# Performance work log

Hardware: AMD Instinct MI355X
Metric: run time of the kernel (lower is better)

The kernel has to match this reference:

```python
import jax, jax.numpy as jnp
import numpy as np

B, Z_DIM, T_DIM, ACT_E, CF, N_ACT, STEPS = 256, 256, 512, 256, 1024, 64, 64


def setup_inputs() -> dict:
    key = jax.random.key(0)
    ks = jax.random.split(key, 12)
    s = 0.02
    def n(k, shape):
        return jax.random.normal(k, shape, jnp.float32) * s
    return {
        "z": jax.random.normal(ks[0], (B, Z_DIM), jnp.float32),
        "W_z2t": n(ks[1], (T_DIM, Z_DIM)), "b_z2t": jnp.zeros((T_DIM,), jnp.float32),
        "E": n(ks[2], (N_ACT, ACT_E)),  # encoder_act2e embedding table
        "Wih_a": n(ks[3], (4 * CF, T_DIM + ACT_E)), "Whh_a": n(ks[4], (4 * CF, CF)),
        "bih_a": jnp.zeros((4 * CF,), jnp.float32), "bhh_a": jnp.zeros((4 * CF,), jnp.float32),
        "Wih_t": n(ks[5], (4 * CF, T_DIM + ACT_E + 1)), "Whh_t": n(ks[6], (4 * CF, CF)),
        "bih_t": jnp.zeros((4 * CF,), jnp.float32), "bhh_t": jnp.zeros((4 * CF,), jnp.float32),
        "W_act": n(ks[7], (N_ACT, CF)), "b_act": jnp.zeros((N_ACT,), jnp.float32),
        "W_ts1": n(ks[8], (CF // 2, CF)), "b_ts1": jnp.zeros((CF // 2,), jnp.float32),
        "W_ts2": n(ks[9], (1, CF // 2)), "b_ts2": jnp.zeros((1,), jnp.float32),
    }


def _lstm_step(x, h, c, Wih, Whh, bih, bhh):
    # PyTorch LSTM gate order: i, f, g, o
    gates = x @ Wih.T + h @ Whh.T + bih + bhh
    i, f, g, o = jnp.split(gates, 4, axis=-1)
    c = jax.nn.sigmoid(f) * c + jax.nn.sigmoid(i) * jnp.tanh(g)
    h = jax.nn.sigmoid(o) * jnp.tanh(c)
    return h, c


def reference(z, W_z2t, b_z2t, E, Wih_a, Whh_a, bih_a, bhh_a,
              Wih_t, Whh_t, bih_t, bhh_t, W_act, b_act,
              W_ts1, b_ts1, W_ts2, b_ts2):
    Bz = z.shape[0]
    t_rec = jax.nn.relu(z @ W_z2t.T + b_z2t)                 # [B, t_dim]
    zeros_h = jnp.zeros((Bz, CF), z.dtype)
    act_emb0 = jnp.broadcast_to(E[-1], (Bz, ACT_E))          # EOT token embedding
    ts0 = jnp.zeros((Bz, 1), z.dtype)

    def step(carry, _):
        h_a, c_a, h_t, c_t, act_emb, ts = carry
        x_a = jnp.concatenate([t_rec, act_emb], axis=1)       # [B, t_dim+act_e]
        h_a, c_a = _lstm_step(x_a, h_a, c_a, Wih_a, Whh_a, bih_a, bhh_a)
        logits = h_a @ W_act.T + b_act                        # [B, num_activities]
        act_emb = E[jnp.argmax(logits, axis=1)]               # [B, act_e]
        x_t = jnp.concatenate([t_rec, act_emb, ts], axis=1)   # [B, t_dim+act_e+1]
        h_t, c_t = _lstm_step(x_t, h_t, c_t, Wih_t, Whh_t, bih_t, bhh_t)
        ts = jax.nn.relu(h_t @ W_ts1.T + b_ts1) @ W_ts2.T + b_ts2  # [B, 1]
        return (h_a, c_a, h_t, c_t, act_emb, ts), (logits, ts)

    carry0 = (zeros_h, zeros_h, zeros_h, zeros_h, act_emb0, ts0)
    _, (logits_seq, ts_seq) = jax.lax.scan(step, carry0, None, length=STEPS)
    acts_rec = jax.nn.softmax(jnp.transpose(logits_seq, (1, 0, 2)), axis=2)  # [B, T, A]
    ts_rec = jnp.transpose(ts_seq[..., 0], (1, 0))                            # [B, T]
    return acts_rec, ts_rec
```

## Files before the change

kernel.cpp:

```cpp
#include <hip/hip_runtime.h>
#include <stdint.h>

typedef unsigned int u32;
typedef float  f32x4 __attribute__((ext_vector_type(4)));
typedef float  f32x2 __attribute__((ext_vector_type(2)));
typedef double f64x2 __attribute__((ext_vector_type(2)));
typedef double f64x4 __attribute__((ext_vector_type(4)));

constexpr int NT  = 256;
constexpr int NTA = 128;
constexpr int BB = 256;
constexpr int ZD = 256;
constexpr int TD = 512;
constexpr int CF = 1024;
constexpr int G4 = 4096;
constexpr int NA = 64;
constexpr int NSTEP = 64;
constexpr int TS_OFF = BB * NSTEP * NA;

constexpr int RSF = 34;
constexpr int FRS = 68;
constexpr int SMEMB = 2 * 64 * RSF * 8;

constexpr int ARS_A = 34;
constexpr int ASZ_A = 32 * ARS_A * 8;
constexpr int BSZ_A = 32 * ARS_A * 4;
constexpr int TRS   = 36;
constexpr int TSZ   = 32 * TRS * 4;
constexpr int SMEMA = (ASZ_A + BSZ_A) > (2 * TSZ) ? (ASZ_A + BSZ_A) : (2 * TSZ);

struct P {
  const float *z, *W_z2t, *b_z2t, *E, *Wih_a, *Whh_a, *bih_a, *bhh_a,
              *Wih_t, *Whh_t, *bih_t, *bhh_t, *W_act, *b_act, *W_ts1, *b_ts1, *W_ts2, *b_ts2;
  float* out;
  double *t_rec64, *pre_a64, *E_proj_a64, *h_a64, *c_a64, *gacc_a;
  float *t_rec32, *pre_t, *E_proj_t, *colt, *h_t, *c_t, *gacc_t, *ts_accum;
  int* idxb;
};

__device__ __forceinline__ float sigf(float x){ return 1.f / (1.f + expf(-x)); }
__device__ __forceinline__ float tanhf_(float x){
  float ax = fabsf(x); float e = expf(-2.f * ax);
  float t = 1.f - 2.f * e / (1.f + e);
  return x < 0.f ? -t : t;
}
__device__ __forceinline__ double sigd(double x){ return 1.0 / (1.0 + exp(-x)); }

__global__ void __launch_bounds__(NT) k_setup(P p){
  __shared__ double sz[ZD];
  const int bid = blockIdx.x, tid = threadIdx.x;
  for (int i = tid; i < ZD; i += NT) sz[i] = (double)p.z[bid * ZD + i];
  __syncthreads();
  for (int k = tid; k < TD; k += NT){
    const float* wr = p.W_z2t + (size_t)k * ZD;
    double a = 0.0;
    for (int j = 0; j < ZD; ++j) a = fma((double)wr[j], sz[j], a);
    a += (double)p.b_z2t[k];
    double t = a > 0.0 ? a : 0.0;
    p.t_rec64[(size_t)bid * TD + k] = t;
    p.t_rec32[(size_t)bid * TD + k] = (float)t;
  }
  for (int i = tid; i < CF; i += NT){
    p.c_a64[(size_t)bid * CF + i] = 0.0;
    p.h_a64[(size_t)bid * CF + i] = 0.0;
    p.c_t[(size_t)bid * CF + i] = 0.f;
    p.h_t[(size_t)bid * CF + i] = 0.f;
  }
  if (tid == 0){ p.idxb[bid] = NA - 1; p.ts_accum[bid] = 0.f; }
}

__global__ void __launch_bounds__(NT) k_eproj(P p){
  __shared__ double sz[ZD];
  const int bid = blockIdx.x, tid = threadIdx.x;
  if (bid < 256){
    const int erow = bid >> 2, cchunk = bid & 3;
    for (int i = tid; i < ZD; i += NT) sz[i] = (double)p.E[erow * ZD + i];
    __syncthreads();
    for (int ci = 0; ci < 4; ++ci){
      const int c = cchunk * 1024 + ci * 256 + tid;
      const float* wr = p.Wih_a + (size_t)c * 768 + 512;
      double a = 0.0;
      for (int j = 0; j < 256; ++j) a = fma((double)wr[j], sz[j], a);
      p.E_proj_a64[(size_t)erow * G4 + c] = a;
    }
  } else if (bid < 512){
    const int erow = (bid - 256) >> 2, cchunk = (bid - 256) & 3;
    for (int i = tid; i < ZD; i += NT) sz[i] = (double)p.E[erow * ZD + i];
    __syncthreads();
    for (int ci = 0; ci < 4; ++ci){
      const int c = cchunk * 1024 + ci * 256 + tid;
      const float* wr = p.Wih_t + (size_t)c * 769 + 512;
      float a = 0.f;
      for (int j = 0; j < 256; ++j) a = fmaf(wr[j], (float)sz[j], a);
      p.E_proj_t[(size_t)erow * G4 + c] = a;
    }
  } else {
    const int c = (bid - 512) * 256 + tid;
    p.colt[c] = p.Wih_t[(size_t)c * 769 + 768];
  }
}

template <bool A64, bool OUT64>
__device__ void mgemm64s(char* smem, const void* __restrict__ Av, int lda,
                         const float* __restrict__ B, int ldb,
                         int rowb, int colb, int K,
                         const float* __restrict__ bih, const float* __restrict__ bhh,
                         void* __restrict__ outv){
  double* As = (double*)smem;
  double* Bs = As + 64 * RSF;
  const int tid = threadIdx.x;
  const int lane = tid & 63;
  const int wm = (tid >> 7) & 1, wn = (tid >> 6) & 1;
  const int m = lane & 15, q = lane >> 4;
  const int tr = tid >> 2, tkq = tid & 3;
  const double* A64p = (const double*)Av;
  const float*  A32p = (const float*)Av;

  double av[8], bv[8];
  auto loadchunk = [&](int kb){
    if (A64){
      const double* ap = A64p + (size_t)(rowb + tr) * lda + kb + tkq * 8;
      #pragma unroll
      for (int j = 0; j < 8; ++j) av[j] = ap[j];
    } else {
      const float* ap = A32p + (size_t)(rowb + tr) * lda + kb + tkq * 8;
      #pragma unroll
      for (int j = 0; j < 8; ++j) av[j] = (double)ap[j];
    }
    const float* bp = B + (size_t)(colb + tr) * ldb + kb + tkq * 8;
    #pragma unroll
    for (int j = 0; j < 8; ++j) bv[j] = (double)bp[j];
  };
  f64x4 acc[2][2];
  #pragma unroll
  for (int g = 0; g < 2; ++g)
    #pragma unroll
    for (int h = 0; h < 2; ++h) acc[g][h] = f64x4{0.0,0.0,0.0,0.0};

  loadchunk(0);
  for (int kb = 0; kb < K; kb += 32){
    __syncthreads();
    {
      double* arow = As + tr * RSF + tkq * 8;
      double* brow = Bs + tr * RSF + tkq * 8;
      #pragma unroll
      for (int j = 0; j < 4; ++j){
        *(f64x2*)(arow + j * 2) = f64x2{av[j], av[j + 4]};
        *(f64x2*)(brow + j * 2) = f64x2{bv[j], bv[j + 4]};
      }
    }
    __syncthreads();
    if (kb + 32 < K) loadchunk(kb + 32);
    #pragma unroll
    for (int sp = 0; sp < 4; ++sp){
      const f64x2 a0 = *(const f64x2*)(As + (wm * 32 +  0 + m) * RSF + sp * 8 + q * 2);
      const f64x2 a1 = *(const f64x2*)(As + (wm * 32 + 16 + m) * RSF + sp * 8 + q * 2);
      const f64x2 b0 = *(const f64x2*)(Bs + (wn * 32 +  0 + m) * RSF + sp * 8 + q * 2);
      const f64x2 b1 = *(const f64x2*)(Bs + (wn * 32 + 16 + m) * RSF + sp * 8 + q * 2);
      acc[0][0] = __builtin_amdgcn_mfma_f64_16x16x4f64(a0[0], b0[0], acc[0][0], 0, 0, 0);
      acc[0][1] = __builtin_amdgcn_mfma_f64_16x16x4f64(a0[0], b1[0], acc[0][1], 0, 0, 0);
      acc[1][0] = __builtin_amdgcn_mfma_f64_16x16x4f64(a1[0], b0[0], acc[1][0], 0, 0, 0);
      acc[1][1] = __builtin_amdgcn_mfma_f64_16x16x4f64(a1[0], b1[0], acc[1][1], 0, 0, 0);
      acc[0][0] = __builtin_amdgcn_mfma_f64_16x16x4f64(a0[1], b0[1], acc[0][0], 0, 0, 0);
      acc[0][1] = __builtin_amdgcn_mfma_f64_16x16x4f64(a0[1], b1[1], acc[0][1], 0, 0, 0);
      acc[1][0] = __builtin_amdgcn_mfma_f64_16x16x4f64(a1[1], b0[1], acc[1][0], 0, 0, 0);
      acc[1][1] = __builtin_amdgcn_mfma_f64_16x16x4f64(a1[1], b1[1], acc[1][1], 0, 0, 0);
    }
  }
  #pragma unroll
  for (int g = 0; g < 2; ++g){
    const int rb = rowb + wm * 32 + g * 16 + q;
    #pragma unroll
    for (int h = 0; h < 2; ++h){
      const int cc = colb + wn * 32 + h * 16 + m;
      const double bb = (double)bih[cc] + (double)bhh[cc];
      #pragma unroll
      for (int v = 0; v < 4; ++v){
        if (OUT64) ((double*)outv)[(size_t)(rb + 4 * v) * G4 + cc] = acc[g][h][v] + bb;
        else       ((float*) outv)[(size_t)(rb + 4 * v) * G4 + cc] = (float)(acc[g][h][v] + bb);
      }
    }
  }
}

__device__ void dgemm32s(char* smem, const float* __restrict__ A, int lda,
                         const float* __restrict__ B, int ldb,
                         int rowb, int colb, int K,
                         const float* __restrict__ bih, const float* __restrict__ bhh,
                         float* __restrict__ outp){
  float* As = (float*)smem;
  float* Bs = (float*)(smem + 64 * FRS * 4);
  const int tid = threadIdx.x;
  const int tx = tid & 15, ty = tid >> 4;
  const int r_ = tid >> 2, kq = tid & 3;
  const int wsw = r_ ^ (kq * 8);
  float acc[4][4];
  #pragma unroll
  for (int i = 0; i < 4; ++i)
    #pragma unroll
    for (int j = 0; j < 4; ++j) acc[i][j] = 0.f;

  float pa[16], pb[16];
  auto ldA = [&](int kb){
    const float* ap = A + (size_t)(rowb + r_) * lda + kb + kq * 16;
    #pragma unroll
    for (int j = 0; j < 16; ++j) pa[j] = ap[j];
  };
  auto ldB = [&](int kb){
    const float* bp = B + (size_t)(colb + r_) * ldb + kb + kq * 16;
    #pragma unroll
    for (int j = 0; j < 16; ++j) pb[j] = bp[j];
  };
  ldA(0); ldB(0);
  for (int kb = 0; kb < K; kb += 64){
    __syncthreads();
    #pragma unroll
    for (int j = 0; j < 16; ++j){
      As[(kq * 16 + j) * FRS + wsw] = pa[j];
      Bs[(kq * 16 + j) * FRS + wsw] = pb[j];
    }
    __syncthreads();
    if (kb + 64 < K){ ldA(kb + 64); ldB(kb + 64); }
    #pragma unroll 4
    for (int k = 0; k < 64; ++k){
      const int sw = (k >> 4) * 8;
      f32x4 a4 = *(const f32x4*)(As + k * FRS + ((4 * ty) ^ sw));
      f32x4 b4 = *(const f32x4*)(Bs + k * FRS + ((4 * tx) ^ sw));
      acc[0][0] = fmaf(a4[0], b4[0], acc[0][0]); acc[0][1] = fmaf(a4[0], b4[1], acc[0][1]);
      acc[0][2] = fmaf(a4[0], b4[2], acc[0][2]); acc[0][3] = fmaf(a4[0], b4[3], acc[0][3]);
      acc[1][0] = fmaf(a4[1], b4[0], acc[1][0]); acc[1][1] = fmaf(a4[1], b4[1], acc[1][1]);
      acc[1][2] = fmaf(a4[1], b4[2], acc[1][2]); acc[1][3] = fmaf(a4[1], b4[3], acc[1][3]);
      acc[2][0] = fmaf(a4[2], b4[0], acc[2][0]); acc[2][1] = fmaf(a4[2], b4[1], acc[2][1]);
      acc[2][2] = fmaf(a4[2], b4[2], acc[2][2]); acc[2][3] = fmaf(a4[2], b4[3], acc[2][3]);
      acc[3][0] = fmaf(a4[3], b4[0], acc[3][0]); acc[3][1] = fmaf(a4[3], b4[1], acc[3][1]);
      acc[3][2] = fmaf(a4[3], b4[2], acc[3][2]); acc[3][3] = fmaf(a4[3], b4[3], acc[3][3]);
    }
  }
  const int c0 = colb + 4 * tx;
  float bb0 = bih[c0+0] + bhh[c0+0], bb1 = bih[c0+1] + bhh[c0+1];
  float bb2 = bih[c0+2] + bhh[c0+2], bb3 = bih[c0+3] + bhh[c0+3];
  #pragma unroll
  for (int i = 0; i < 4; ++i){
    float* o = outp + (size_t)(rowb + 4 * ty + i) * G4 + c0;
    o[0] = acc[i][0] + bb0; o[1] = acc[i][1] + bb1;
    o[2] = acc[i][2] + bb2; o[3] = acc[i][3] + bb3;
  }
}

__device__ void mgemm64w(char* smem, const double* __restrict__ A, int lda,
                         const float* __restrict__ B, int ldb,
                         int rowb, int colb, int K,
                         const double* __restrict__ addin, double* __restrict__ outp){
  double* As = (double*)smem;
  float*  Bs = (float*)(smem + ASZ_A);
  const int tid = threadIdx.x, lane = tid & 63;
  const int w = tid >> 6;
  const int m = lane & 15, q = lane >> 4;
  const int tr = tid >> 2, tkq = tid & 3;
  double av[8]; float bv[8];
  auto loadchunk = [&](int kb){
    const double* ap = A + (size_t)(rowb + tr) * lda + kb + tkq * 8;
    #pragma unroll
    for (int j = 0; j < 8; ++j) av[j] = ap[j];
    const float* bp = B + (size_t)(colb + tr) * ldb + kb + tkq * 8;
    #pragma unroll
    for (int j = 0; j < 8; ++j) bv[j] = bp[j];
  };
  f64x4 acc0{0,0,0,0}, acc1{0,0,0,0};
  loadchunk(0);
  for (int kb = 0; kb < K; kb += 32){
    __syncthreads();
    {
      double* arow = As + tr * ARS_A + tkq * 8;
      float*  brow = Bs + tr * ARS_A + tkq * 8;
      #pragma unroll
      for (int j = 0; j < 4; ++j){
        *(f64x2*)(arow + j * 2) = f64x2{av[j], av[j + 4]};
        *(f32x2*)(brow + j * 2) = f32x2{bv[j], bv[j + 4]};
      }
    }
    __syncthreads();
    if (kb + 32 < K) loadchunk(kb + 32);
    #pragma unroll
    for (int sp = 0; sp < 4; ++sp){
      const f64x2 a0  = *(const f64x2*)(As + (16 * w + m) * ARS_A + sp * 8 + q * 2);
      const f32x2 b0f = *(const f32x2*)(Bs + ( 0 + m) * ARS_A + sp * 8 + q * 2);
      const f32x2 b1f = *(const f32x2*)(Bs + (16 + m) * ARS_A + sp * 8 + q * 2);
      acc0 = __builtin_amdgcn_mfma_f64_16x16x4f64(a0[0], (double)b0f[0], acc0, 0, 0, 0);
      acc1 = __builtin_amdgcn_mfma_f64_16x16x4f64(a0[0], (double)b1f[0], acc1, 0, 0, 0);
      acc0 = __builtin_amdgcn_mfma_f64_16x16x4f64(a0[1], (double)b0f[1], acc0, 0, 0, 0);
      acc1 = __builtin_amdgcn_mfma_f64_16x16x4f64(a0[1], (double)b1f[1], acc1, 0, 0, 0);
    }
  }
  const int rb = rowb + 16 * w + q;
  #pragma unroll
  for (int h = 0; h < 2; ++h){
    const f64x4 a = h ? acc1 : acc0;
    const int cc = colb + h * 16 + m;
    #pragma unroll
    for (int v = 0; v < 4; ++v){
      const size_t o = (size_t)(rb + 4 * v) * G4 + cc;
      outp[o] = a[v] + addin[o];
    }
  }
}

__device__ void dgemm32w(char* smem, const float* __restrict__ A, int lda,
                         const float* __restrict__ B, int ldb,
                         int rowb, int colb, int K,
                         const float* __restrict__ addin, float* __restrict__ outp){
  float* As = (float*)smem;
  float* Bs = (float*)(smem + TSZ);
  const int tid = threadIdx.x;
  const int tx = tid & 7, ty = tid >> 3;
  const int r_ = tid >> 2, kq = tid & 3;
  const int wsw = r_ ^ (kq * 8);
  float acc[2][4];
  #pragma unroll
  for (int i = 0; i < 2; ++i)
    #pragma unroll
    for (int j = 0; j < 4; ++j) acc[i][j] = 0.f;
  float pa[8], pb[8];
  auto ldAB = [&](int kb){
    const float* ap = A + (size_t)(rowb + r_) * lda + kb + kq * 8;
    #pragma unroll
    for (int j = 0; j < 8; ++j) pa[j] = ap[j];
    const float* bp = B + (size_t)(colb + r_) * ldb + kb + kq * 8;
    #pragma unroll
    for (int j = 0; j < 8; ++j) pb[j] = bp[j];
  };
  ldAB(0);
  for (int kb = 0; kb < K; kb += 32){
    __syncthreads();
    #pragma unroll
    for (int j = 0; j < 8; ++j){
      As[(kq * 8 + j) * TRS + wsw] = pa[j];
      Bs[(kq * 8 + j) * TRS + wsw] = pb[j];
    }
    __syncthreads();
    if (kb + 32 < K) ldAB(kb + 32);
    #pragma unroll 4
    for (int k = 0; k < 32; ++k){
      const int sw = (k >> 3) * 8;
      f32x2 a2 = *(const f32x2*)(As + k * TRS + ((2 * ty) ^ sw));
      f32x4 b4 = *(const f32x4*)(Bs + k * TRS + ((4 * tx) ^ sw));
      acc[0][0] = fmaf(a2[0], b4[0], acc[0][0]); acc[0][1] = fmaf(a2[0], b4[1], acc[0][1]);
      acc[0][2] = fmaf(a2[0], b4[2], acc[0][2]); acc[0][3] = fmaf(a2[0], b4[3], acc[0][3]);
      acc[1][0] = fmaf(a2[1], b4[0], acc[1][0]); acc[1][1] = fmaf(a2[1], b4[1], acc[1][1]);
      acc[1][2] = fmaf(a2[1], b4[2], acc[1][2]); acc[1][3] = fmaf(a2[1], b4[3], acc[1][3]);
    }
  }
  const int c0 = colb + 4 * tx;
  #pragma unroll
  for (int i = 0; i < 2; ++i){
    const size_t base = (size_t)(rowb + 2 * ty + i) * G4 + c0;
    const float* ai = addin + base;
    float* o = outp + base;
    o[0] = acc[i][0] + ai[0]; o[1] = acc[i][1] + ai[1];
    o[2] = acc[i][2] + ai[2]; o[3] = acc[i][3] + ai[3];
  }
}

__device__ void tshead_j(const P& p, int bid, int hbuf){
  const int tid = threadIdx.x;
  const int tm = bid >> 6, tjq = bid & 63;
  const int rowb = tm * 32;
  const int rt = tid >> 3, j8 = tid & 7;
  const int j = tjq * 8 + j8;
  const float* __restrict__ hr = p.h_t + (size_t)hbuf * BB * CF + (size_t)(rowb + rt) * CF;
  const float* __restrict__ wr = p.W_ts1 + (size_t)j * CF;
  float a0=0,a1=0,a2=0,a3=0;
  for (int k = 0; k < CF; k += 16){
    f32x4 h0 = *(const f32x4*)(hr + k),     h1 = *(const f32x4*)(hr + k + 4);
    f32x4 h2 = *(const f32x4*)(hr + k + 8), h3 = *(const f32x4*)(hr + k + 12);
    f32x4 w0 = *(const f32x4*)(wr + k),     w1 = *(const f32x4*)(wr + k + 4);
    f32x4 w2 = *(const f32x4*)(wr + k + 8), w3 = *(const f32x4*)(wr + k + 12);
    a0 = fmaf(h0[0],w0[0], fmaf(h0[1],w0[1], fmaf(h0[2],w0[2], fmaf(h0[3],w0[3], a0))));
    a1 = fmaf(h1[0],w1[0], fmaf(h1[1],w1[1], fmaf(h1[2],w1[2], fmaf(h1[3],w1[3], a1))));
    a2 = fmaf(h2[0],w2[0], fmaf(h2[1],w2[1], fmaf(h2[2],w2[2], fmaf(h2[3],w2[3], a2))));
    a3 = fmaf(h3[0],w3[0], fmaf(h3[1],w3[1], fmaf(h3[2],w3[2], fmaf(h3[3],w3[3], a3))));
  }
  float v = ((a0 + a1) + (a2 + a3)) + p.b_ts1[j];
  v = (v > 0.f ? v : 0.f) * p.W_ts2[j];
  v += __shfl_xor(v, 1, 64);
  v += __shfl_xor(v, 2, 64);
  v += __shfl_xor(v, 4, 64);
  if (j8 == 0) atomicAdd(p.ts_accum + rowb + rt, v);
}

__device__ void tshead_j128(const P& p, int bid, int hbuf){
  const int tid = threadIdx.x;
  const int tm = bid >> 7, tjq = bid & 127;
  const int rowb = tm * 32;
  const int rt = tid >> 2, j4 = tid & 3;
  const int j = tjq * 4 + j4;
  const float* __restrict__ hr = p.h_t + (size_t)hbuf * BB * CF + (size_t)(rowb + rt) * CF;
  const float* __restrict__ wr = p.W_ts1 + (size_t)j * CF;
  float a0=0,a1=0,a2=0,a3=0;
  for (int k = 0; k < CF; k += 16){
    f32x4 h0 = *(const f32x4*)(hr + k),     h1 = *(const f32x4*)(hr + k + 4);
    f32x4 h2 = *(const f32x4*)(hr + k + 8), h3 = *(const f32x4*)(hr + k + 12);
    f32x4 w0 = *(const f32x4*)(wr + k),     w1 = *(const f32x4*)(wr + k + 4);
    f32x4 w2 = *(const f32x4*)(wr + k + 8), w3 = *(const f32x4*)(wr + k + 12);
    a0 = fmaf(h0[0],w0[0], fmaf(h0[1],w0[1], fmaf(h0[2],w0[2], fmaf(h0[3],w0[3], a0))));
    a1 = fmaf(h1[0],w1[0], fmaf(h1[1],w1[1], fmaf(h1[2],w1[2], fmaf(h1[3],w1[3], a1))));
    a2 = fmaf(h2[0],w2[0], fmaf(h2[1],w2[1], fmaf(h2[2],w2[2], fmaf(h2[3],w2[3], a2))));
    a3 = fmaf(h3[0],w3[0], fmaf(h3[1],w3[1], fmaf(h3[2],w3[2], fmaf(h3[3],w3[3], a3))));
  }
  float v = ((a0 + a1) + (a2 + a3)) + p.b_ts1[j];
  v = (v > 0.f ? v : 0.f) * p.W_ts2[j];
  v += __shfl_xor(v, 1, 64);
  v += __shfl_xor(v, 2, 64);
  if (j4 == 0) atomicAdd(p.ts_accum + rowb + rt, v);
}

__global__ void __launch_bounds__(NT) k_pre(P p){
  __shared__ __align__(16) char smem[SMEMB];
  const int bid = blockIdx.x;
  const int hsel = bid >> 8, sub = bid & 255;
  const int rowb = (sub >> 6) * 64, colb = (sub & 63) * 64;
  if (hsel == 0)
    mgemm64s<true, true>(smem, p.t_rec64, TD, p.Wih_a, 768, rowb, colb, TD,
                         p.bih_a, p.bhh_a, p.pre_a64);
  else
    dgemm32s(smem, p.t_rec32, TD, p.Wih_t, 769, rowb, colb, TD,
             p.bih_t, p.bhh_t, p.pre_t);
}

__global__ void __launch_bounds__(NTA) k_stepA(P p, int s){
  __shared__ __align__(16) char smem[SMEMA];
  const int bid = blockIdx.x;
  if (s > 0 && bid < 1024) tshead_j128(p, bid, s & 1);
  const int hsel = bid >> 10, sub = bid & 1023;
  const int rowb = (sub >> 7) * 32, colb = (sub & 127) * 32;
  const int rd = s & 1;
  if (hsel == 0)
    mgemm64w(smem, p.h_a64 + (size_t)rd * BB * CF, CF, p.Whh_a, CF,
             rowb, colb, CF, p.pre_a64, p.gacc_a);
  else
    dgemm32w(smem, p.h_t + (size_t)rd * BB * CF, CF, p.Whh_t, CF,
             rowb, colb, CF, p.pre_t, p.gacc_t);
}

__global__ void __launch_bounds__(NT) k_stepB(P p, int s){
  __shared__ double shd[1092];
  const int b = blockIdx.x, tid = threadIdx.x;
  const int cur = (s + 1) & 1;
  int idxp = p.idxb[b];
  idxp = idxp < 0 ? 0 : (idxp > 63 ? 63 : idxp);
  {
    const double* ga = p.gacc_a + (size_t)b * G4;
    const double* ea = p.E_proj_a64 + (size_t)idxp * G4;
    const int c0 = tid * 4;
    #pragma unroll
    for (int jj = 0; jj < 4; ++jj){
      const int c = c0 + jj;
      double gi = ga[0*CF + c] + ea[0*CF + c];
      double gf = ga[1*CF + c] + ea[1*CF + c];
      double gg = ga[2*CF + c] + ea[2*CF + c];
      double go = ga[3*CF + c] + ea[3*CF + c];
      double cv = p.c_a64[(size_t)b * CF + c];
      double cn = sigd(gf) * cv + sigd(gi) * tanh(gg);
      double hn = sigd(go) * tanh(cn);
      p.c_a64[(size_t)b * CF + c] = cn;
      p.h_a64[(size_t)cur * BB * CF + (size_t)b * CF + c] = hn;
      shd[c] = hn;
    }
  }
  if (tid == 0) shd[1088] = (s == 0) ? 0.0 : ((double)p.ts_accum[b] + (double)p.b_ts2[0]);
  __syncthreads();
  {
    const int w = tid >> 6, l = tid & 63, l15 = l & 15, quad = l >> 4;
    const int a = w * 16 + l15;
    const float* wr = p.W_act + (size_t)a * CF + quad * 256;
    const double* hp = shd + quad * 256;
    double acc = 0.0;
    for (int kk = 0; kk < 256; kk += 4){
      acc = fma((double)wr[kk+0], hp[kk+0], acc);
      acc = fma((double)wr[kk+1], hp[kk+1], acc);
      acc = fma((double)wr[kk+2], hp[kk+2], acc);
      acc = fma((double)wr[kk+3], hp[kk+3], acc);
    }
    acc += __shfl_xor(acc, 16, 64);
    acc += __shfl_xor(acc, 32, 64);
    if (quad == 0) shd[1024 + a] = acc;
  }
  __syncthreads();
  if (tid < 64){
    double acc = shd[1024 + tid] + (double)p.b_act[tid];
    double m = acc;
    #pragma unroll
    for (int off = 32; off; off >>= 1) m = fmax(m, __shfl_xor(m, off, 64));
    unsigned long long ball = __ballot(acc == m);
    int idxv = __ffsll(ball) - 1;
    idxv = idxv < 0 ? 0 : (idxv > 63 ? 63 : idxv);
    double e = exp(acc - m);
    double ssum = e;
    #pragma unroll
    for (int off = 32; off; off >>= 1) ssum += __shfl_xor(ssum, off, 64);
    p.out[(size_t)b * (NSTEP * NA) + s * NA + tid] = (float)(e / ssum);
    if (tid == 0){
      p.idxb[b] = idxv;
      shd[1089] = (double)idxv;
      if (s > 0) p.out[TS_OFF + b * NSTEP + (s - 1)] = (float)shd[1088];
    }
  }
  __syncthreads();
  const float ts_val = (float)shd[1088];
  const int idxv = (int)shd[1089];
  const int c0 = tid * 4;
  const float* gb = p.gacc_t   + (size_t)b * G4;
  const float* eb = p.E_proj_t + (size_t)idxv * G4;
  f32x4 gi = *(const f32x4*)(gb + 0*CF + c0) + *(const f32x4*)(eb + 0*CF + c0) + ts_val * *(const f32x4*)(p.colt + 0*CF + c0);
  f32x4 gf = *(const f32x4*)(gb + 1*CF + c0) + *(const f32x4*)(eb + 1*CF + c0) + ts_val * *(const f32x4*)(p.colt + 1*CF + c0);
  f32x4 gg = *(const f32x4*)(gb + 2*CF + c0) + *(const f32x4*)(eb + 2*CF + c0) + ts_val * *(const f32x4*)(p.colt + 2*CF + c0);
  f32x4 go = *(const f32x4*)(gb + 3*CF + c0) + *(const f32x4*)(eb + 3*CF + c0) + ts_val * *(const f32x4*)(p.colt + 3*CF + c0);
  f32x4 cv = *(f32x4*)(p.c_t + (size_t)b * CF + c0);
  f32x4 cn, hn;
  #pragma unroll
  for (int jj = 0; jj < 4; ++jj){
    float cj = sigf(gf[jj]) * cv[jj] + sigf(gi[jj]) * tanhf_(gg[jj]);
    float hj = sigf(go[jj]) * tanhf_(cj);
    cn[jj] = cj; hn[jj] = hj;
  }
  *(f32x4*)(p.c_t + (size_t)b * CF + c0) = cn;
  *(f32x4*)(p.h_t + (size_t)cur * BB * CF + (size_t)b * CF + c0) = hn;
  __syncthreads();
  if (tid == 0) p.ts_accum[b] = 0.f;
}

__global__ void __launch_bounds__(NT) k_tsfin(P p){
  tshead_j(p, blockIdx.x, 0);
}
__global__ void __launch_bounds__(NT) k_tswrite(P p){
  p.out[TS_OFF + threadIdx.x * NSTEP + 63] = p.ts_accum[threadIdx.x] + p.b_ts2[0];
}

extern "C" void kernel_launch(void* const* d_in, const int* in_sizes, int n_in,
                              void* d_out, int out_size, void* d_ws, size_t ws_size,
                              hipStream_t stream){
  (void)in_sizes; (void)n_in; (void)out_size; (void)ws_size;
  P p;
  p.z     = (const float*)d_in[0];  p.W_z2t = (const float*)d_in[1];  p.b_z2t = (const float*)d_in[2];
  p.E     = (const float*)d_in[3];  p.Wih_a = (const float*)d_in[4];  p.Whh_a = (const float*)d_in[5];
  p.bih_a = (const float*)d_in[6];  p.bhh_a = (const float*)d_in[7];  p.Wih_t = (const float*)d_in[8];
  p.Whh_t = (const float*)d_in[9];  p.bih_t = (const float*)d_in[10]; p.bhh_t = (const float*)d_in[11];
  p.W_act = (const float*)d_in[12]; p.b_act = (const float*)d_in[13]; p.W_ts1 = (const float*)d_in[14];
  p.b_ts1 = (const float*)d_in[15]; p.W_ts2 = (const float*)d_in[16]; p.b_ts2 = (const float*)d_in[17];
  p.out = (float*)d_out;
  char* w = (char*)d_ws;
  size_t off = 0;
  auto alloc = [&](size_t bytes) -> void* { void* r = w + off; off += (bytes + 255) & ~(size_t)255; return r; };
  p.t_rec64    = (double*)alloc((size_t)BB * TD * 8);
  p.pre_a64    = (double*)alloc((size_t)BB * G4 * 8);
  p.E_proj_a64 = (double*)alloc((size_t)NA * G4 * 8);
  p.h_a64      = (double*)alloc((size_t)2 * BB * CF * 8);
  p.c_a64      = (double*)alloc((size_t)BB * CF * 8);
  p.gacc_a     = (double*)alloc((size_t)BB * G4 * 8);
  p.t_rec32    = (float*)alloc((size_t)BB * TD * 4);
  p.pre_t      = (float*)alloc((size_t)BB * G4 * 4);
  p.E_proj_t   = (float*)alloc((size_t)NA * G4 * 4);
  p.colt       = (float*)alloc((size_t)G4 * 4);
  p.h_t        = (float*)alloc((size_t)2 * BB * CF * 4);
  p.c_t        = (float*)alloc((size_t)BB * CF * 4);
  p.gacc_t     = (float*)alloc((size_t)BB * G4 * 4);
  p.ts_accum   = (float*)alloc((size_t)BB * 4);
  p.idxb       = (int*)  alloc((size_t)BB * 4);

  k_setup<<<dim3(256), dim3(NT), 0, stream>>>(p);
  k_eproj<<<dim3(528), dim3(NT), 0, stream>>>(p);
  k_pre  <<<dim3(512), dim3(NT), 0, stream>>>(p);
  for (int s = 0; s < NSTEP; ++s){
    k_stepA<<<dim3(2048), dim3(NTA), 0, stream>>>(p, s);
    k_stepB<<<dim3(256),  dim3(NT),  0, stream>>>(p, s);
  }
  k_tsfin  <<<dim3(512), dim3(NT), 0, stream>>>(p);
  k_tswrite<<<dim3(1),   dim3(NT), 0, stream>>>(p);
}
```

Before: 10.10 ms.

## Shrink recurrent GEMM row tiles to 16 and double stepA grid

Result: slower. 12.89 ms (+27.6%).

```diff
diff --git a/kernel.cpp b/kernel.cpp
--- a/kernel.cpp
+++ b/kernel.cpp
@@ -23,7 +23,7 @@
 constexpr int SMEMB = 2 * 64 * RSF * 8;
 
 constexpr int ARS_A = 34;
-constexpr int ASZ_A = 32 * ARS_A * 8;
+constexpr int ASZ_A = 16 * ARS_A * 8;
 constexpr int BSZ_A = 32 * ARS_A * 4;
 constexpr int TRS   = 36;
 constexpr int TSZ   = 32 * TRS * 4;
@@ -247,7 +247,7 @@
   }
 }
 
-__device__ void mgemm64w(char* smem, const double* __restrict__ A, int lda,
+__device__ void mgemm16w(char* smem, const double* __restrict__ A, int lda,
                          const float* __restrict__ B, int ldb,
                          int rowb, int colb, int K,
                          const double* __restrict__ addin, double* __restrict__ outp){
@@ -259,53 +259,51 @@
   const int tr = tid >> 2, tkq = tid & 3;
   double av[8]; float bv[8];
   auto loadchunk = [&](int kb){
-    const double* ap = A + (size_t)(rowb + tr) * lda + kb + tkq * 8;
-    #pragma unroll
-    for (int j = 0; j < 8; ++j) av[j] = ap[j];
+    if (tid < 64){
+      const double* ap = A + (size_t)(rowb + tr) * lda + kb + tkq * 8;
+      #pragma unroll
+      for (int j = 0; j < 8; ++j) av[j] = ap[j];
+    }
     const float* bp = B + (size_t)(colb + tr) * ldb + kb + tkq * 8;
     #pragma unroll
     for (int j = 0; j < 8; ++j) bv[j] = bp[j];
   };
-  f64x4 acc0{0,0,0,0}, acc1{0,0,0,0};
+  f64x4 acc{0,0,0,0};
   loadchunk(0);
   for (int kb = 0; kb < K; kb += 32){
     __syncthreads();
     {
-      double* arow = As + tr * ARS_A + tkq * 8;
-      float*  brow = Bs + tr * ARS_A + tkq * 8;
-      #pragma unroll
-      for (int j = 0; j < 4; ++j){
-        *(f64x2*)(arow + j * 2) = f64x2{av[j], av[j + 4]};
+      float* brow = Bs + tr * ARS_A + tkq * 8;
+      #pragma unroll
+      for (int j = 0; j < 4; ++j)
         *(f32x2*)(brow + j * 2) = f32x2{bv[j], bv[j + 4]};
+      if (tid < 64){
+        double* arow = As + tr * ARS_A + tkq * 8;
+        #pragma unroll
+        for (int j = 0; j < 4; ++j)
+          *(f64x2*)(arow + j * 2) = f64x2{av[j], av[j + 4]};
       }
     }
     __syncthreads();
     if (kb + 32 < K) loadchunk(kb + 32);
     #pragma unroll
     for (int sp = 0; sp < 4; ++sp){
-      const f64x2 a0  = *(const f64x2*)(As + (16 * w + m) * ARS_A + sp * 8 + q * 2);
-      const f32x2 b0f = *(const f32x2*)(Bs + ( 0 + m) * ARS_A + sp * 8 + q * 2);
-      const f32x2 b1f = *(const f32x2*)(Bs + (16 + m) * ARS_A + sp * 8 + q * 2);
-      acc0 = __builtin_amdgcn_mfma_f64_16x16x4f64(a0[0], (double)b0f[0], acc0, 0, 0, 0);
-      acc1 = __builtin_amdgcn_mfma_f64_16x16x4f64(a0[0], (double)b1f[0], acc1, 0, 0, 0);
-      acc0 = __builtin_amdgcn_mfma_f64_16x16x4f64(a0[1], (double)b0f[1], acc0, 0, 0, 0);
-      acc1 = __builtin_amdgcn_mfma_f64_16x16x4f64(a0[1], (double)b1f[1], acc1, 0, 0, 0);
-    }
-  }
-  const int rb = rowb + 16 * w + q;
-  #pragma unroll
-  for (int h = 0; h < 2; ++h){
-    const f64x4 a = h ? acc1 : acc0;
-    const int cc = colb + h * 16 + m;
-    #pragma unroll
-    for (int v = 0; v < 4; ++v){
-      const size_t o = (size_t)(rb + 4 * v) * G4 + cc;
-      outp[o] = a[v] + addin[o];
-    }
-  }
-}
-
-__device__ void dgemm32w(char* smem, const float* __restrict__ A, int lda,
+      const f64x2 a0  = *(const f64x2*)(As + m * ARS_A + sp * 8 + q * 2);
+      const f32x2 b0f = *(const f32x2*)(Bs + (16 * w + m) * ARS_A + sp * 8 + q * 2);
+      acc = __builtin_amdgcn_mfma_f64_16x16x4f64(a0[0], (double)b0f[0], acc, 0, 0, 0);
+      acc = __builtin_amdgcn_mfma_f64_16x16x4f64(a0[1], (double)b0f[1], acc, 0, 0, 0);
+    }
+  }
+  const int rb = rowb + q;
+  const int cc = colb + 16 * w + m;
+  #pragma unroll
+  for (int v = 0; v < 4; ++v){
+    const size_t o = (size_t)(rb + 4 * v) * G4 + cc;
+    outp[o] = acc[v] + addin[o];
+  }
+}
+
+__device__ void dgemm16w(char* smem, const float* __restrict__ A, int lda,
                          const float* __restrict__ B, int ldb,
                          int rowb, int colb, int K,
                          const float* __restrict__ addin, float* __restrict__ outp){
@@ -315,16 +313,16 @@
   const int tx = tid & 7, ty = tid >> 3;
   const int r_ = tid >> 2, kq = tid & 3;
   const int wsw = r_ ^ (kq * 8);
-  float acc[2][4];
-  #pragma unroll
-  for (int i = 0; i < 2; ++i)
-    #pragma unroll
-    for (int j = 0; j < 4; ++j) acc[i][j] = 0.f;
+  float acc[4];
+  #pragma unroll
+  for (int j = 0; j < 4; ++j) acc[j] = 0.f;
   float pa[8], pb[8];
   auto ldAB = [&](int kb){
-    const float* ap = A + (size_t)(rowb + r_) * lda + kb + kq * 8;
-    #pragma unroll
-    for (int j = 0; j < 8; ++j) pa[j] = ap[j];
+    if (tid < 64){
+      const float* ap = A + (size_t)(rowb + r_) * lda + kb + kq * 8;
+      #pragma unroll
+      for (int j = 0; j < 8; ++j) pa[j] = ap[j];
+    }
     const float* bp = B + (size_t)(colb + r_) * ldb + kb + kq * 8;
     #pragma unroll
     for (int j = 0; j < 8; ++j) pb[j] = bp[j];
@@ -333,32 +331,30 @@
   for (int kb = 0; kb < K; kb += 32){
     __syncthreads();
     #pragma unroll
-    for (int j = 0; j < 8; ++j){
-      As[(kq * 8 + j) * TRS + wsw] = pa[j];
+    for (int j = 0; j < 8; ++j)
       Bs[(kq * 8 + j) * TRS + wsw] = pb[j];
+    if (tid < 64){
+      #pragma unroll
+      for (int j = 0; j < 8; ++j)
+        As[(kq * 8 + j) * TRS + wsw] = pa[j];
     }
     __syncthreads();
     if (kb + 32 < K) ldAB(kb + 32);
     #pragma unroll 4
     for (int k = 0; k < 32; ++k){
       const int sw = (k >> 3) * 8;
-      f32x2 a2 = *(const f32x2*)(As + k * TRS + ((2 * ty) ^ sw));
+      const float a = As[k * TRS + (ty ^ sw)];
       f32x4 b4 = *(const f32x4*)(Bs + k * TRS + ((4 * tx) ^ sw));
-      acc[0][0] = fmaf(a2[0], b4[0], acc[0][0]); acc[0][1] = fmaf(a2[0], b4[1], acc[0][1]);
-      acc[0][2] = fmaf(a2[0], b4[2], acc[0][2]); acc[0][3] = fmaf(a2[0], b4[3], acc[0][3]);
-      acc[1][0] = fmaf(a2[1], b4[0], acc[1][0]); acc[1][1] = fmaf(a2[1], b4[1], acc[1][1]);
-      acc[1][2] = fmaf(a2[1], b4[2], acc[1][2]); acc[1][3] = fmaf(a2[1], b4[3], acc[1][3]);
+      acc[0] = fmaf(a, b4[0], acc[0]); acc[1] = fmaf(a, b4[1], acc[1]);
+      acc[2] = fmaf(a, b4[2], acc[2]); acc[3] = fmaf(a, b4[3], acc[3]);
     }
   }
   const int c0 = colb + 4 * tx;
-  #pragma unroll
-  for (int i = 0; i < 2; ++i){
-    const size_t base = (size_t)(rowb + 2 * ty + i) * G4 + c0;
-    const float* ai = addin + base;
-    float* o = outp + base;
-    o[0] = acc[i][0] + ai[0]; o[1] = acc[i][1] + ai[1];
-    o[2] = acc[i][2] + ai[2]; o[3] = acc[i][3] + ai[3];
-  }
+  const size_t base = (size_t)(rowb + ty) * G4 + c0;
+  const float* ai = addin + base;
+  float* o = outp + base;
+  o[0] = acc[0] + ai[0]; o[1] = acc[1] + ai[1];
+  o[2] = acc[2] + ai[2]; o[3] = acc[3] + ai[3];
 }
 
 __device__ void tshead_j(const P& p, int bid, int hbuf){
@@ -431,14 +427,14 @@
   __shared__ __align__(16) char smem[SMEMA];
   const int bid = blockIdx.x;
   if (s > 0 && bid < 1024) tshead_j128(p, bid, s & 1);
-  const int hsel = bid >> 10, sub = bid & 1023;
-  const int rowb = (sub >> 7) * 32, colb = (sub & 127) * 32;
+  const int hsel = bid >> 11, sub = bid & 2047;
+  const int rowb = (sub >> 7) * 16, colb = (sub & 127) * 32;
   const int rd = s & 1;
   if (hsel == 0)
-    mgemm64w(smem, p.h_a64 + (size_t)rd * BB * CF, CF, p.Whh_a, CF,
+    mgemm16w(smem, p.h_a64 + (size_t)rd * BB * CF, CF, p.Whh_a, CF,
              rowb, colb, CF, p.pre_a64, p.gacc_a);
   else
-    dgemm32w(smem, p.h_t + (size_t)rd * BB * CF, CF, p.Whh_t, CF,
+    dgemm16w(smem, p.h_t + (size_t)rd * BB * CF, CF, p.Whh_t, CF,
              rowb, colb, CF, p.pre_t, p.gacc_t);
 }
 
@@ -571,7 +567,7 @@
   k_eproj<<<dim3(528), dim3(NT), 0, stream>>>(p);
   k_pre  <<<dim3(512), dim3(NT), 0, stream>>>(p);
   for (int s = 0; s < NSTEP; ++s){
-    k_stepA<<<dim3(2048), dim3(NTA), 0, stream>>>(p, s);
+    k_stepA<<<dim3(4096), dim3(NTA), 0, stream>>>(p, s);
     k_stepB<<<dim3(256),  dim3(NT),  0, stream>>>(p, s);
   }
   k_tsfin  <<<dim3(512), dim3(NT), 0, stream>>>(p);
```
